# Performance work log

Measured on AMD Instinct MI355X. Metric: run time of the kernel, lower is better.

## Reference

```python
import jax, jax.numpy as jnp
import numpy as np

D_MODEL = 256
NUM_HEADS = 4
D_HEAD = D_MODEL // NUM_HEADS
LN_EPS = 1e-5
NEG_INF = -1e9


def setup_inputs() -> dict:
    key = jax.random.key(0)
    ks = jax.random.split(key, 8)
    B, N = 4, 2048
    s = 1.0 / np.sqrt(D_MODEL)
    return {
        "x": jax.random.normal(ks[0], (B, N, D_MODEL), dtype=jnp.float32),
        "Wq": jax.random.normal(ks[1], (D_MODEL, D_MODEL), dtype=jnp.float32) * s,
        "Wk": jax.random.normal(ks[2], (D_MODEL, D_MODEL), dtype=jnp.float32) * s,
        "Wv": jax.random.normal(ks[3], (D_MODEL, D_MODEL), dtype=jnp.float32) * s,
        "Wo": jax.random.normal(ks[4], (D_MODEL, D_MODEL), dtype=jnp.float32) * s,
        "bo": jnp.zeros((D_MODEL,), dtype=jnp.float32),
        "gamma": jnp.ones((D_MODEL,), dtype=jnp.float32),
        "beta": jnp.zeros((D_MODEL,), dtype=jnp.float32),
        "k_neighbors": 8,
    }


def build_knn_adj(x, k):
    # x: [B, N, D]; returns symmetric 0/1 adjacency [B, N, N]
    B, N, _ = x.shape
    xn = x / jnp.maximum(jnp.linalg.norm(x, axis=-1, keepdims=True), 1e-12)
    sim = jnp.einsum('bnd,bmd->bnm', xn, xn)  # [B, N, N]
    _, idx = jax.lax.top_k(sim, k + 1)        # [B, N, k+1]
    b = jnp.arange(B)[:, None, None]
    r = jnp.arange(N)[None, :, None]
    adj = jnp.zeros((B, N, N), dtype=jnp.float32).at[b, r, idx].add(1.0)
    adj = jnp.maximum(adj, jnp.swapaxes(adj, 1, 2))
    return adj


def layer_norm(x, gamma, beta):
    mu = jnp.mean(x, axis=-1, keepdims=True)
    var = jnp.mean(jnp.square(x - mu), axis=-1, keepdims=True)
    return (x - mu) * jax.lax.rsqrt(var + LN_EPS) * gamma + beta


def reference(x, Wq, Wk, Wv, Wo, bo, gamma, beta, k_neighbors):
    B, N, D = x.shape
    adj = build_knn_adj(x, k_neighbors)  # [B, N, N]

    def split_heads(t):  # [B, N, D] -> [B, H, N, d]
        return jnp.transpose(t.reshape(B, N, NUM_HEADS, D_HEAD), (0, 2, 1, 3))

    q = split_heads(x @ Wq)
    k = split_heads(x @ Wk)
    v = split_heads(x @ Wv)

    scores = jnp.einsum('bhnd,bhmd->bhnm', q, k) / jnp.sqrt(jnp.float32(D_HEAD))
    scores = jnp.where(adj[:, None, :, :] > 0, scores, NEG_INF)
    attn = jax.nn.softmax(scores, axis=-1)  # dropout is identity at inference
    out = jnp.einsum('bhnm,bhmd->bhnd', attn, v)
    out = jnp.transpose(out, (0, 2, 1, 3)).reshape(B, N, D)
    out = out @ Wo + bo
    return layer_norm(x + out, gamma, beta)
```

## Files before the change

kernel.cpp:

```cpp
#include <hip/hip_runtime.h>
#include <hip/hip_bf16.h>
#include <math.h>

#define BATCH 4
#define N 2048
#define D 256
#define NH 4
#define DH 64
#define TOPK 9
#define NEG_BIG -1e30f

typedef __bf16 bf16;
typedef __bf16 bf16x8 __attribute__((ext_vector_type(8)));
typedef float f32x4 __attribute__((ext_vector_type(4)));

#define PK3(a,b,c) ((a) | ((b) << 2) | ((c) << 4))
#define PK6(a,b,c,d,e,f) ((a) | ((b) << 2) | ((c) << 4) | ((d) << 6) | ((e) << 8) | ((f) << 10))

#define WAITVM(Nc) __builtin_amdgcn_s_waitcnt((((Nc) & 0xf)) | (7u << 4) | (0xfu << 8) | ((((unsigned)(Nc)) >> 4) << 14))

__device__ __forceinline__ void async_cp16(const bf16* g, const bf16* l) {
  __builtin_amdgcn_global_load_lds(
      (const __attribute__((address_space(1))) void*)(uintptr_t)g,
      (__attribute__((address_space(3))) void*)(uintptr_t)l, 16, 0, 0);
}

__global__ __launch_bounds__(64) void prep_kernel(const float* __restrict__ x,
                                                  const float* __restrict__ Wq,
                                                  const float* __restrict__ Wk,
                                                  const float* __restrict__ Wv,
                                                  const float* __restrict__ Wo,
                                                  bf16* __restrict__ XsN,
                                                  bf16* __restrict__ Wt,
                                                  float* __restrict__ norms,
                                                  uint4* __restrict__ mask4) {
  int blk = blockIdx.x;
  int lane = threadIdx.x;
  if (blk < 8192) {
    float4 v = *(const float4*)(x + (size_t)blk * D + lane * 4);
    float ss = v.x * v.x + v.y * v.y + v.z * v.z + v.w * v.w;
    for (int off = 32; off; off >>= 1) ss += __shfl_down(ss, off);
    ss = __shfl(ss, 0);
    float nrm = fmaxf(sqrtf(ss), 1e-12f);
    if (lane == 0) norms[blk] = nrm;
    float sc = 1.0f / nrm;
    float xs[4] = {v.x * sc, v.y * sc, v.z * sc, v.w * sc};
    bf16* o = XsN + (size_t)blk * 768 + lane * 4;
#pragma unroll
    for (int j = 0; j < 4; ++j) {
      float xv = xs[j];
      bf16 h = (bf16)xv;
      float r1 = xv - (float)h;
      bf16 m = (bf16)r1;
      o[j] = h;
      o[256 + j] = m;
      o[512 + j] = (bf16)(r1 - (float)m);
    }
  } else if (blk < 9216) {
    int jj = blk - 8192;
    const float* W = (jj < 256) ? Wq : (jj < 512) ? Wk : (jj < 768) ? Wv : Wo;
    int j = jj & 255;
    bf16* dst = Wt + (size_t)jj * 512;
    for (int k = lane; k < 256; k += 64) {
      float w = W[(size_t)k * D + j];
      bf16 h = (bf16)w;
      dst[k] = h;
      dst[256 + k] = (bf16)(w - (float)h);
    }
  } else {
    int base = (blk - 9216) * 1024 + lane;
#pragma unroll
    for (int t = 0; t < 16; ++t)
      mask4[base + t * 64] = make_uint4(0, 0, 0, 0);
  }
}

__device__ __forceinline__ void gemm_core(bf16* As, bf16* Bs,
                                          const bf16* __restrict__ Ab,
                                          const bf16* __restrict__ Bb,
                                          float* __restrict__ Cb,
                                          int lda, int ldb, int ldc,
                                          int nsteps, int amap, int bmap,
                                          int row0, int col0,
                                          bool mirror, bool nt,
                                          const float* __restrict__ rowscale) {
  int tid = threadIdx.x;
  int lane = tid & 63;
  int wv = tid >> 6;
  int wm = (wv >> 1) * 64;
  int wn = (wv & 1) * 64;

  int rbase = tid >> 3;
  int gperm = (tid & 7) ^ (rbase & 7);
  const bf16* ga0 = Ab + (size_t)rbase * lda + gperm * 8;
  const bf16* gb0 = Bb + (size_t)rbase * ldb + gperm * 8;
  int ldsoff = tid * 8;

  int fr = lane & 15;
  int fq = (lane >> 4) * 8;

  f32x4 acc[4][4] = {};

  auto issue = [&](int st, int buf) {
    int ch = st >> 2;
    int aoff = (((amap >> (ch * 2)) & 3) << 8) | ((st & 3) << 6);
    int boff = (((bmap >> (ch * 2)) & 3) << 8) | ((st & 3) << 6);
#pragma unroll
    for (int q = 0; q < 4; ++q)
      async_cp16(ga0 + (size_t)q * 32 * lda + aoff, &As[buf * 8192 + ldsoff + q * 2048]);
#pragma unroll
    for (int q = 0; q < 4; ++q)
      async_cp16(gb0 + (size_t)q * 32 * ldb + boff, &Bs[buf * 8192 + ldsoff + q * 2048]);
  };

  issue(0, 0);
  for (int st = 0; st < nsteps; ++st) {
    int buf = st & 1;
    if (st + 1 < nsteps) {
      issue(st + 1, buf ^ 1);
      WAITVM(8);
    } else {
      WAITVM(0);
    }
    __builtin_amdgcn_s_barrier();
#pragma unroll
    for (int ks = 0; ks < 64; ks += 32) {
      bf16x8 af[4], bfr[4];
#pragma unroll
      for (int mi = 0; mi < 4; ++mi) {
        int r = wm + mi * 16 + fr;
        int G = (ks + fq) >> 3;
        af[mi] = *(const bf16x8*)&As[buf * 8192 + r * 64 + ((G ^ (r & 7)) << 3)];
      }
#pragma unroll
      for (int nj = 0; nj < 4; ++nj) {
        int r = wn + nj * 16 + fr;
        int G = (ks + fq) >> 3;
        bfr[nj] = *(const bf16x8*)&Bs[buf * 8192 + r * 64 + ((G ^ (r & 7)) << 3)];
      }
#pragma unroll
      for (int mi = 0; mi < 4; ++mi)
#pragma unroll
        for (int nj = 0; nj < 4; ++nj)
          acc[mi][nj] = __builtin_amdgcn_mfma_f32_16x16x32_bf16(af[mi], bfr[nj], acc[mi][nj], 0, 0, 0);
    }
    __builtin_amdgcn_s_barrier();
  }

  int er = (lane >> 4) * 4;
  int ec = lane & 15;
#pragma unroll
  for (int mi = 0; mi < 4; ++mi) {
    int rb = row0 + wm + mi * 16 + er;
    float scl[4] = {1.f, 1.f, 1.f, 1.f};
    if (rowscale) {
      float4 s4 = *(const float4*)(rowscale + rb);
      scl[0] = s4.x; scl[1] = s4.y; scl[2] = s4.z; scl[3] = s4.w;
    }
#pragma unroll
    for (int nj = 0; nj < 4; ++nj) {
      int cb = col0 + wn + nj * 16 + ec;
      if (nt) {
#pragma unroll
        for (int reg = 0; reg < 4; ++reg)
          __builtin_nontemporal_store(acc[mi][nj][reg],
                                      &Cb[(size_t)(rb + reg) * ldc + cb]);
        if (mirror) {
#pragma unroll
          for (int reg = 0; reg < 4; ++reg)
            __builtin_nontemporal_store(acc[mi][nj][reg],
                                        &Cb[(size_t)cb * ldc + rb + reg]);
        }
      } else {
#pragma unroll
        for (int reg = 0; reg < 4; ++reg)
          Cb[(size_t)(rb + reg) * ldc + cb] = acc[mi][nj][reg] * scl[reg];
      }
    }
  }
}

__global__ __launch_bounds__(256) void gemm_sim_kernel(const bf16* __restrict__ XsN,
                                                       float* __restrict__ sim,
                                                       int amap, int bmap) {
  __shared__ bf16 As[2 * 128 * 64];
  __shared__ bf16 Bs[2 * 128 * 64];
  int g = blockIdx.x;
  int xcd = g & 7;
  int slot = g >> 3;
  int z = xcd >> 1;
  int t = (xcd & 1) * 68 + slot;
  int by = 0;
  while (t >= 16 - by) { t -= 16 - by; ++by; }
  int bx = by + t;
  gemm_core(As, Bs,
            XsN + (size_t)z * N * 768 + (size_t)by * 128 * 768,
            XsN + (size_t)z * N * 768 + (size_t)bx * 128 * 768,
            sim + (size_t)z * N * N,
            768, 768, N, 12, amap, bmap, by * 128, bx * 128,
            bx != by, true, nullptr);
}

__global__ __launch_bounds__(256) void gemm_gen_kernel(const bf16* __restrict__ A,
                                                       const bf16* __restrict__ B,
                                                       float* __restrict__ C,
                                                       int lda, int ldb, int ldc,
                                                       int nsteps, int amap, int bmap,
                                                       const float* __restrict__ rowscale) {
  __shared__ bf16 As[2 * 128 * 64];
  __shared__ bf16 Bs[2 * 128 * 64];
  gemm_core(As, Bs,
            A + (size_t)blockIdx.y * 128 * lda,
            B + (size_t)blockIdx.x * 128 * ldb,
            C, lda, ldb, ldc, nsteps, amap, bmap,
            blockIdx.y * 128, blockIdx.x * 128, false, false, rowscale);
}

__global__ __launch_bounds__(256) void gemm_fused_kernel(const bf16* __restrict__ XsN,
                                                         float* __restrict__ sim,
                                                         int amap_s, int bmap_s,
                                                         const bf16* __restrict__ Wt,
                                                         float* __restrict__ qkv,
                                                         int amap_q, int bmap_q,
                                                         const float* __restrict__ norms) {
  __shared__ bf16 As[2 * 128 * 64];
  __shared__ bf16 Bs[2 * 128 * 64];
  int g = blockIdx.x;
  if (g < 544) {
    int xcd = g & 7;
    int slot = g >> 3;
    int z = xcd >> 1;
    int t = (xcd & 1) * 68 + slot;
    int by = 0;
    while (t >= 16 - by) { t -= 16 - by; ++by; }
    int bx = by + t;
    gemm_core(As, Bs,
              XsN + (size_t)z * N * 768 + (size_t)by * 128 * 768,
              XsN + (size_t)z * N * 768 + (size_t)bx * 128 * 768,
              sim + (size_t)z * N * N,
              768, 768, N, 12, amap_s, bmap_s, by * 128, bx * 128,
              bx != by, true, nullptr);
  } else {
    int t = g - 544;
    int bx = t % 6;
    int by = t / 6;
    gemm_core(As, Bs,
              XsN + (size_t)by * 128 * 768,
              Wt + (size_t)bx * 128 * 512,
              qkv, 768, 512, 768, 8, amap_q, bmap_q,
              by * 128, bx * 128, false, false, norms);
  }
}

__global__ __launch_bounds__(64) void topk_adj_kernel(const float* __restrict__ sim,
                                                      unsigned* __restrict__ mask) {
  int row = blockIdx.x;
  int lane = threadIdx.x;
  int b = row >> 11, r = row & 2047;
  const float* srow = sim + (size_t)row * N;
  float v[32];
#pragma unroll
  for (int it = 0; it < 8; ++it) {
    float4 q = *(const float4*)(srow + it * 256 + lane * 4);
    v[it * 4 + 0] = q.x; v[it * 4 + 1] = q.y;
    v[it * 4 + 2] = q.z; v[it * 4 + 3] = q.w;
  }
  unsigned removed = 0;
  for (int rs = 0; rs < TOPK; ++rs) {
    float m = -3e38f;
    int mi = 0;
#pragma unroll
    for (int i = 0; i < 32; ++i) {
      float vv = ((removed >> i) & 1u) ? -3e38f : v[i];
      if (vv > m) { m = vv; mi = i; }
    }
    int gidx = ((mi >> 2) << 8) + lane * 4 + (mi & 3);
    for (int off = 32; off; off >>= 1) {
      float om = __shfl_down(m, off);
      int og = __shfl_down(gidx, off);
      if (om > m || (om == m && og < gidx)) { m = om; gidx = og; }
    }
    gidx = __shfl(gidx, 0);
    if (((gidx >> 2) & 63) == lane)
      removed |= 1u << (((gidx >> 8) << 2) | (gidx & 3));
    if (lane == 0) {
      atomicOr(&mask[(size_t)row * 64 + (gidx >> 5)], 1u << (gidx & 31));
      atomicOr(&mask[(((size_t)b << 11) + gidx) * 64 + (r >> 5)], 1u << (r & 31));
    }
  }
}

__global__ __launch_bounds__(256) void attn_kernel(const float* __restrict__ qkv,
                                                   const unsigned* __restrict__ mask,
                                                   bf16* __restrict__ aos) {
  __shared__ float sq[4][256];
  __shared__ unsigned short nbr[4][2048];
  __shared__ int s_nn[4];
  int wv = threadIdx.x >> 6;
  int lane = threadIdx.x & 63;
  int g = blockIdx.x;
  int xcd = g & 7;
  int b = xcd >> 1;
  int tile = (xcd & 1) * 256 + (g >> 3);
  int bn = b * N + tile * 4 + wv;
  if (lane == 0) s_nn[wv] = 0;
  *(float4*)&sq[wv][lane * 4] = *(const float4*)(qkv + (size_t)bn * 768 + lane * 4);
  __syncthreads();
  unsigned bits = mask[(size_t)bn * (N / 32) + lane];
  while (bits) {
    int bit = __ffs(bits) - 1;
    bits &= bits - 1;
    int p = atomicAdd(&s_nn[wv], 1);
    nbr[wv][p] = (unsigned short)(lane * 32 + bit);
  }
  __syncthreads();
  int nn = s_nn[wv];
  const float* base = qkv + (size_t)b * N * 768;
  float acc[4] = {0.f, 0.f, 0.f, 0.f};

  auto score4 = [&](int j, float* s) {
    const float* kr = base + (size_t)j * 768 + 256;
#pragma unroll
    for (int h = 0; h < 4; ++h) {
      float a = 0.f;
#pragma unroll
      for (int c = 0; c < DH; c += 4) {
        float4 kk = *(const float4*)(kr + h * DH + c);
        a += sq[wv][h * DH + c] * kk.x + sq[wv][h * DH + c + 1] * kk.y +
             sq[wv][h * DH + c + 2] * kk.z + sq[wv][h * DH + c + 3] * kk.w;
      }
      s[h] = a * 0.125f;
    }
  };

  if (nn <= 64) {
    float s[4] = {NEG_BIG, NEG_BIG, NEG_BIG, NEG_BIG};
    if (lane < nn) score4(nbr[wv][lane], s);
    float w[4], l[4];
#pragma unroll
    for (int h = 0; h < 4; ++h) {
      float m = s[h];
      for (int off = 32; off; off >>= 1) m = fmaxf(m, __shfl_down(m, off));
      m = __shfl(m, 0);
      float e = (lane < nn) ? __expf(s[h] - m) : 0.f;
      float ls = e;
      for (int off = 32; off; off >>= 1) ls += __shfl_down(ls, off);
      l[h] = __shfl(ls, 0);
      w[h] = e;
    }
    int i = 0;
    for (; i + 4 <= nn; i += 4) {
      int j0 = nbr[wv][i + 0], j1 = nbr[wv][i + 1];
      int j2 = nbr[wv][i + 2], j3 = nbr[wv][i + 3];
      const float* p0 = base + (size_t)j0 * 768 + 512;
      const float* p1 = base + (size_t)j1 * 768 + 512;
      const float* p2 = base + (size_t)j2 * 768 + 512;
      const float* p3 = base + (size_t)j3 * 768 + 512;
#pragma unroll
      for (int h = 0; h < 4; ++h) {
        acc[h] += __shfl(w[h], i + 0) * p0[h * DH + lane] +
                  __shfl(w[h], i + 1) * p1[h * DH + lane] +
                  __shfl(w[h], i + 2) * p2[h * DH + lane] +
                  __shfl(w[h], i + 3) * p3[h * DH + lane];
      }
    }
    for (; i < nn; ++i) {
      const float* p0 = base + (size_t)nbr[wv][i] * 768 + 512;
#pragma unroll
      for (int h = 0; h < 4; ++h) acc[h] += __shfl(w[h], i) * p0[h * DH + lane];
    }
#pragma unroll
    for (int h = 0; h < 4; ++h) acc[h] /= l[h];
  } else {
    float m[4] = {NEG_BIG, NEG_BIG, NEG_BIG, NEG_BIG};
    for (int i0 = 0; i0 < nn; i0 += 64) {
      float s[4] = {NEG_BIG, NEG_BIG, NEG_BIG, NEG_BIG};
      if (i0 + lane < nn) score4(nbr[wv][i0 + lane], s);
#pragma unroll
      for (int h = 0; h < 4; ++h) m[h] = fmaxf(m[h], s[h]);
    }
#pragma unroll
    for (int h = 0; h < 4; ++h) {
      for (int off = 32; off; off >>= 1) m[h] = fmaxf(m[h], __shfl_down(m[h], off));
      m[h] = __shfl(m[h], 0);
    }
    float l[4] = {0.f, 0.f, 0.f, 0.f};
    for (int i0 = 0; i0 < nn; i0 += 64) {
      float s[4] = {NEG_BIG, NEG_BIG, NEG_BIG, NEG_BIG};
      if (i0 + lane < nn) score4(nbr[wv][i0 + lane], s);
      float e[4];
#pragma unroll
      for (int h = 0; h < 4; ++h) {
        e[h] = (i0 + lane < nn) ? __expf(s[h] - m[h]) : 0.f;
        float ls = e[h];
        for (int off = 32; off; off >>= 1) ls += __shfl_down(ls, off);
        l[h] += __shfl(ls, 0);
      }
      int lim = min(64, nn - i0);
      for (int ii = 0; ii < lim; ++ii) {
        const float* p0 = base + (size_t)nbr[wv][i0 + ii] * 768 + 512;
#pragma unroll
        for (int h = 0; h < 4; ++h) acc[h] += __shfl(e[h], ii) * p0[h * DH + lane];
      }
    }
#pragma unroll
    for (int h = 0; h < 4; ++h) acc[h] /= l[h];
  }
#pragma unroll
  for (int h = 0; h < 4; ++h) {
    float a = acc[h];
    bf16 hi = (bf16)a;
    aos[(size_t)bn * 512 + h * DH + lane] = hi;
    aos[(size_t)bn * 512 + 256 + h * DH + lane] = (bf16)(a - (float)hi);
  }
}

__global__ __launch_bounds__(64) void ln_kernel(const float* __restrict__ x,
                                                const float* __restrict__ proj,
                                                const float* __restrict__ bo,
                                                const float* __restrict__ gamma,
                                                const float* __restrict__ beta,
                                                float* __restrict__ out) {
  int row = blockIdx.x;
  int lane = threadIdx.x;
  size_t base = (size_t)row * D + lane * 4;
  float4 xv = *(const float4*)(x + base);
  float4 pv = *(const float4*)(proj + base);
  float4 bv = *(const float4*)(bo + lane * 4);
  float u0 = xv.x + pv.x + bv.x, u1 = xv.y + pv.y + bv.y;
  float u2 = xv.z + pv.z + bv.z, u3 = xv.w + pv.w + bv.w;
  float s = u0 + u1 + u2 + u3;
  for (int off = 32; off; off >>= 1) s += __shfl_down(s, off);
  s = __shfl(s, 0);
  float mean = s * (1.0f / D);
  float d0 = u0 - mean, d1 = u1 - mean, d2 = u2 - mean, d3 = u3 - mean;
  float ss = d0 * d0 + d1 * d1 + d2 * d2 + d3 * d3;
  for (int off = 32; off; off >>= 1) ss += __shfl_down(ss, off);
  ss = __shfl(ss, 0);
  float rstd = rsqrtf(ss * (1.0f / D) + 1e-5f);
  float4 gv = *(const float4*)(gamma + lane * 4);
  float4 be = *(const float4*)(beta + lane * 4);
  float4 o;
  o.x = d0 * rstd * gv.x + be.x;
  o.y = d1 * rstd * gv.y + be.y;
  o.z = d2 * rstd * gv.z + be.z;
  o.w = d3 * rstd * gv.w + be.w;
  *(float4*)(out + base) = o;
}

extern "C" void kernel_launch(void* const* d_in, const int* in_sizes, int n_in,
                              void* d_out, int out_size, void* d_ws, size_t ws_size,
                              hipStream_t stream) {
  const float* x     = (const float*)d_in[0];
  const float* Wq    = (const float*)d_in[1];
  const float* Wk    = (const float*)d_in[2];
  const float* Wv    = (const float*)d_in[3];
  const float* Wo    = (const float*)d_in[4];
  const float* bo    = (const float*)d_in[5];
  const float* gamma = (const float*)d_in[6];
  const float* beta  = (const float*)d_in[7];
  float* out = (float*)d_out;

  char* ws = (char*)d_ws;
  bf16* XsN      = (bf16*)(ws);
  float* sim     = (float*)(ws + 12582912);
  float* norms   = (float*)(ws + 79691776);
  unsigned* mask = (unsigned*)(ws + 79986688);
  bf16* Wt       = (bf16*)(ws + 82083840);

  bool big = ws_size >= (size_t)125075456;
  float* qkv  = (float*)(ws + (big ? 83132416  : 12582912));
  bf16* aos   = (bf16*)(ws + (big ? 108298240 : 37748736));
  float* proj = (float*)(ws + (big ? 116686848 : 46137344));

  const int AMAP_SIM = PK6(0, 0, 1, 0, 0, 0);
  const int BMAP_SIM = PK6(0, 1, 0, 0, 0, 0);
  const int AMAP_2T  = PK3(0, 1, 0);
  const int BMAP_2T  = PK3(0, 0, 1);

  prep_kernel<<<9344, 64, 0, stream>>>(x, Wq, Wk, Wv, Wo, XsN, Wt, norms,
                                       (uint4*)mask);

  if (big) {
    gemm_fused_kernel<<<928, 256, 0, stream>>>(
        XsN, sim, AMAP_SIM, BMAP_SIM, Wt, qkv, AMAP_2T, BMAP_2T, norms);
    topk_adj_kernel<<<BATCH * N, 64, 0, stream>>>(sim, mask);
  } else {
    gemm_sim_kernel<<<544, 256, 0, stream>>>(XsN, sim, AMAP_SIM, BMAP_SIM);
    topk_adj_kernel<<<BATCH * N, 64, 0, stream>>>(sim, mask);
    gemm_gen_kernel<<<dim3(6, 64), 256, 0, stream>>>(
        XsN, Wt, qkv, 768, 512, 768, 8, AMAP_2T, BMAP_2T, norms);
  }

  attn_kernel<<<(BATCH * N) / 4, 256, 0, stream>>>(qkv, mask, aos);

  gemm_gen_kernel<<<dim3(2, 64), 256, 0, stream>>>(
      aos, Wt + (size_t)768 * 512, proj, 512, 512, D, 8, AMAP_2T, BMAP_2T, nullptr);
  ln_kernel<<<BATCH * N, 64, 0, stream>>>(x, proj, bo, gamma, beta, out);
}
```

Before: 198.7 us.

## Store QKV in bf16, shrink the normalized-x split, and fuse out-projection with LayerNorm

The normalized-x representation drops from a three-term bf16 split to a two-term split. That shrinks the buffer and its stride, though the sim GEMM keeps its step count. The QKV GEMM now writes bf16 instead of fp32, which halves the gather traffic in the attention kernel, where K and V are converted on load. The output projection GEMM and the LayerNorm kernel are merged into one projln kernel. Each block computes a full 128x256 row tile and reduces the row statistics in LDS, so the fp32 proj intermediate and one launch disappear. In exchange, precision drops for the similarity scores, which can change top-k selection, and for Q/K/V. The fused kernel also launches only 64 blocks, which leaves most compute units idle.

```diff
diff --git a/kernel.cpp b/kernel.cpp
--- a/kernel.cpp
+++ b/kernel.cpp
@@ -11,6 +11,7 @@
 #define NEG_BIG -1e30f
 
 typedef __bf16 bf16;
+typedef __bf16 bf16x4 __attribute__((ext_vector_type(4)));
 typedef __bf16 bf16x8 __attribute__((ext_vector_type(8)));
 typedef float f32x4 __attribute__((ext_vector_type(4)));
 
@@ -45,16 +46,13 @@
     if (lane == 0) norms[blk] = nrm;
     float sc = 1.0f / nrm;
     float xs[4] = {v.x * sc, v.y * sc, v.z * sc, v.w * sc};
-    bf16* o = XsN + (size_t)blk * 768 + lane * 4;
+    bf16* o = XsN + (size_t)blk * 512 + lane * 4;
 #pragma unroll
     for (int j = 0; j < 4; ++j) {
       float xv = xs[j];
       bf16 h = (bf16)xv;
-      float r1 = xv - (float)h;
-      bf16 m = (bf16)r1;
       o[j] = h;
-      o[256 + j] = m;
-      o[512 + j] = (bf16)(r1 - (float)m);
+      o[256 + j] = (bf16)(xv - (float)h);
     }
   } else if (blk < 9216) {
     int jj = blk - 8192;
@@ -78,11 +76,11 @@
 __device__ __forceinline__ void gemm_core(bf16* As, bf16* Bs,
                                           const bf16* __restrict__ Ab,
                                           const bf16* __restrict__ Bb,
-                                          float* __restrict__ Cb,
+                                          void* __restrict__ Cvoid,
                                           int lda, int ldb, int ldc,
                                           int nsteps, int amap, int bmap,
                                           int row0, int col0,
-                                          bool mirror, bool nt,
+                                          int outmode, bool mirror,
                                           const float* __restrict__ rowscale) {
   int tid = threadIdx.x;
   int lane = tid & 63;
@@ -160,7 +158,8 @@
 #pragma unroll
     for (int nj = 0; nj < 4; ++nj) {
       int cb = col0 + wn + nj * 16 + ec;
-      if (nt) {
+      if (outmode == 1) {
+        float* Cb = (float*)Cvoid;
 #pragma unroll
         for (int reg = 0; reg < 4; ++reg)
           __builtin_nontemporal_store(acc[mi][nj][reg],
@@ -172,9 +171,10 @@
                                         &Cb[(size_t)cb * ldc + rb + reg]);
         }
       } else {
+        bf16* Cb = (bf16*)Cvoid;
 #pragma unroll
         for (int reg = 0; reg < 4; ++reg)
-          Cb[(size_t)(rb + reg) * ldc + cb] = acc[mi][nj][reg] * scl[reg];
+          Cb[(size_t)(rb + reg) * ldc + cb] = (bf16)(acc[mi][nj][reg] * scl[reg]);
       }
     }
   }
@@ -194,33 +194,32 @@
   while (t >= 16 - by) { t -= 16 - by; ++by; }
   int bx = by + t;
   gemm_core(As, Bs,
-            XsN + (size_t)z * N * 768 + (size_t)by * 128 * 768,
-            XsN + (size_t)z * N * 768 + (size_t)bx * 128 * 768,
+            XsN + (size_t)z * N * 512 + (size_t)by * 128 * 512,
+            XsN + (size_t)z * N * 512 + (size_t)bx * 128 * 512,
             sim + (size_t)z * N * N,
-            768, 768, N, 12, amap, bmap, by * 128, bx * 128,
-            bx != by, true, nullptr);
-}
-
-__global__ __launch_bounds__(256) void gemm_gen_kernel(const bf16* __restrict__ A,
-                                                       const bf16* __restrict__ B,
-                                                       float* __restrict__ C,
-                                                       int lda, int ldb, int ldc,
-                                                       int nsteps, int amap, int bmap,
-                                                       const float* __restrict__ rowscale) {
+            512, 512, N, 12, amap, bmap, by * 128, bx * 128,
+            1, bx != by, nullptr);
+}
+
+__global__ __launch_bounds__(256) void gemm_qkv_kernel(const bf16* __restrict__ XsN,
+                                                       const bf16* __restrict__ Wt,
+                                                       bf16* __restrict__ qkv,
+                                                       int amap, int bmap,
+                                                       const float* __restrict__ norms) {
   __shared__ bf16 As[2 * 128 * 64];
   __shared__ bf16 Bs[2 * 128 * 64];
   gemm_core(As, Bs,
-            A + (size_t)blockIdx.y * 128 * lda,
-            B + (size_t)blockIdx.x * 128 * ldb,
-            C, lda, ldb, ldc, nsteps, amap, bmap,
-            blockIdx.y * 128, blockIdx.x * 128, false, false, rowscale);
+            XsN + (size_t)blockIdx.y * 128 * 512,
+            Wt + (size_t)blockIdx.x * 128 * 512,
+            qkv, 512, 512, 768, 8, amap, bmap,
+            blockIdx.y * 128, blockIdx.x * 128, 2, false, norms);
 }
 
 __global__ __launch_bounds__(256) void gemm_fused_kernel(const bf16* __restrict__ XsN,
                                                          float* __restrict__ sim,
                                                          int amap_s, int bmap_s,
                                                          const bf16* __restrict__ Wt,
-                                                         float* __restrict__ qkv,
+                                                         bf16* __restrict__ qkv,
                                                          int amap_q, int bmap_q,
                                                          const float* __restrict__ norms) {
   __shared__ bf16 As[2 * 128 * 64];
@@ -235,20 +234,20 @@
     while (t >= 16 - by) { t -= 16 - by; ++by; }
     int bx = by + t;
     gemm_core(As, Bs,
-              XsN + (size_t)z * N * 768 + (size_t)by * 128 * 768,
-              XsN + (size_t)z * N * 768 + (size_t)bx * 128 * 768,
+              XsN + (size_t)z * N * 512 + (size_t)by * 128 * 512,
+              XsN + (size_t)z * N * 512 + (size_t)bx * 128 * 512,
               sim + (size_t)z * N * N,
-              768, 768, N, 12, amap_s, bmap_s, by * 128, bx * 128,
-              bx != by, true, nullptr);
+              512, 512, N, 12, amap_s, bmap_s, by * 128, bx * 128,
+              1, bx != by, nullptr);
   } else {
     int t = g - 544;
     int bx = t % 6;
     int by = t / 6;
     gemm_core(As, Bs,
-              XsN + (size_t)by * 128 * 768,
+              XsN + (size_t)by * 128 * 512,
               Wt + (size_t)bx * 128 * 512,
-              qkv, 768, 512, 768, 8, amap_q, bmap_q,
-              by * 128, bx * 128, false, false, norms);
+              qkv, 512, 512, 768, 8, amap_q, bmap_q,
+              by * 128, bx * 128, 2, false, norms);
   }
 }
 
@@ -290,7 +289,7 @@
   }
 }
 
-__global__ __launch_bounds__(256) void attn_kernel(const float* __restrict__ qkv,
+__global__ __launch_bounds__(256) void attn_kernel(const bf16* __restrict__ qkv,
                                                    const unsigned* __restrict__ mask,
                                                    bf16* __restrict__ aos) {
   __shared__ float sq[4][256];
@@ -304,7 +303,11 @@
   int tile = (xcd & 1) * 256 + (g >> 3);
   int bn = b * N + tile * 4 + wv;
   if (lane == 0) s_nn[wv] = 0;
-  *(float4*)&sq[wv][lane * 4] = *(const float4*)(qkv + (size_t)bn * 768 + lane * 4);
+  {
+    bf16x4 qv = *(const bf16x4*)(qkv + (size_t)bn * 768 + lane * 4);
+#pragma unroll
+    for (int j = 0; j < 4; ++j) sq[wv][lane * 4 + j] = (float)qv[j];
+  }
   __syncthreads();
   unsigned bits = mask[(size_t)bn * (N / 32) + lane];
   while (bits) {
@@ -315,19 +318,19 @@
   }
   __syncthreads();
   int nn = s_nn[wv];
-  const float* base = qkv + (size_t)b * N * 768;
+  const bf16* base = qkv + (size_t)b * N * 768;
   float acc[4] = {0.f, 0.f, 0.f, 0.f};
 
   auto score4 = [&](int j, float* s) {
-    const float* kr = base + (size_t)j * 768 + 256;
+    const bf16* kr = base + (size_t)j * 768 + 256;
 #pragma unroll
     for (int h = 0; h < 4; ++h) {
       float a = 0.f;
 #pragma unroll
-      for (int c = 0; c < DH; c += 4) {
-        float4 kk = *(const float4*)(kr + h * DH + c);
-        a += sq[wv][h * DH + c] * kk.x + sq[wv][h * DH + c + 1] * kk.y +
-             sq[wv][h * DH + c + 2] * kk.z + sq[wv][h * DH + c + 3] * kk.w;
+      for (int c = 0; c < DH; c += 8) {
+        bf16x8 kk = *(const bf16x8*)(kr + h * DH + c);
+#pragma unroll
+        for (int t = 0; t < 8; ++t) a += sq[wv][h * DH + c + t] * (float)kk[t];
       }
       s[h] = a * 0.125f;
     }
@@ -352,22 +355,22 @@
     for (; i + 4 <= nn; i += 4) {
       int j0 = nbr[wv][i + 0], j1 = nbr[wv][i + 1];
       int j2 = nbr[wv][i + 2], j3 = nbr[wv][i + 3];
-      const float* p0 = base + (size_t)j0 * 768 + 512;
-      const float* p1 = base + (size_t)j1 * 768 + 512;
-      const float* p2 = base + (size_t)j2 * 768 + 512;
-      const float* p3 = base + (size_t)j3 * 768 + 512;
+      const bf16* p0 = base + (size_t)j0 * 768 + 512;
+      const bf16* p1 = base + (size_t)j1 * 768 + 512;
+      const bf16* p2 = base + (size_t)j2 * 768 + 512;
+      const bf16* p3 = base + (size_t)j3 * 768 + 512;
 #pragma unroll
       for (int h = 0; h < 4; ++h) {
-        acc[h] += __shfl(w[h], i + 0) * p0[h * DH + lane] +
-                  __shfl(w[h], i + 1) * p1[h * DH + lane] +
-                  __shfl(w[h], i + 2) * p2[h * DH + lane] +
-                  __shfl(w[h], i + 3) * p3[h * DH + lane];
+        acc[h] += __shfl(w[h], i + 0) * (float)p0[h * DH + lane] +
+                  __shfl(w[h], i + 1) * (float)p1[h * DH + lane] +
+                  __shfl(w[h], i + 2) * (float)p2[h * DH + lane] +
+                  __shfl(w[h], i + 3) * (float)p3[h * DH + lane];
       }
     }
     for (; i < nn; ++i) {
-      const float* p0 = base + (size_t)nbr[wv][i] * 768 + 512;
-#pragma unroll
-      for (int h = 0; h < 4; ++h) acc[h] += __shfl(w[h], i) * p0[h * DH + lane];
+      const bf16* p0 = base + (size_t)nbr[wv][i] * 768 + 512;
+#pragma unroll
+      for (int h = 0; h < 4; ++h) acc[h] += __shfl(w[h], i) * (float)p0[h * DH + lane];
     }
 #pragma unroll
     for (int h = 0; h < 4; ++h) acc[h] /= l[h];
@@ -398,9 +401,9 @@
       }
       int lim = min(64, nn - i0);
       for (int ii = 0; ii < lim; ++ii) {
-        const float* p0 = base + (size_t)nbr[wv][i0 + ii] * 768 + 512;
-#pragma unroll
-        for (int h = 0; h < 4; ++h) acc[h] += __shfl(e[h], ii) * p0[h * DH + lane];
+        const bf16* p0 = base + (size_t)nbr[wv][i0 + ii] * 768 + 512;
+#pragma unroll
+        for (int h = 0; h < 4; ++h) acc[h] += __shfl(e[h], ii) * (float)p0[h * DH + lane];
       }
     }
 #pragma unroll
@@ -415,37 +418,120 @@
   }
 }
 
-__global__ __launch_bounds__(64) void ln_kernel(const float* __restrict__ x,
-                                                const float* __restrict__ proj,
-                                                const float* __restrict__ bo,
-                                                const float* __restrict__ gamma,
-                                                const float* __restrict__ beta,
-                                                float* __restrict__ out) {
-  int row = blockIdx.x;
-  int lane = threadIdx.x;
-  size_t base = (size_t)row * D + lane * 4;
-  float4 xv = *(const float4*)(x + base);
-  float4 pv = *(const float4*)(proj + base);
-  float4 bv = *(const float4*)(bo + lane * 4);
-  float u0 = xv.x + pv.x + bv.x, u1 = xv.y + pv.y + bv.y;
-  float u2 = xv.z + pv.z + bv.z, u3 = xv.w + pv.w + bv.w;
-  float s = u0 + u1 + u2 + u3;
-  for (int off = 32; off; off >>= 1) s += __shfl_down(s, off);
-  s = __shfl(s, 0);
-  float mean = s * (1.0f / D);
-  float d0 = u0 - mean, d1 = u1 - mean, d2 = u2 - mean, d3 = u3 - mean;
-  float ss = d0 * d0 + d1 * d1 + d2 * d2 + d3 * d3;
-  for (int off = 32; off; off >>= 1) ss += __shfl_down(ss, off);
-  ss = __shfl(ss, 0);
-  float rstd = rsqrtf(ss * (1.0f / D) + 1e-5f);
-  float4 gv = *(const float4*)(gamma + lane * 4);
-  float4 be = *(const float4*)(beta + lane * 4);
-  float4 o;
-  o.x = d0 * rstd * gv.x + be.x;
-  o.y = d1 * rstd * gv.y + be.y;
-  o.z = d2 * rstd * gv.z + be.z;
-  o.w = d3 * rstd * gv.w + be.w;
-  *(float4*)(out + base) = o;
+__global__ __launch_bounds__(256) void projln_kernel(const bf16* __restrict__ A,
+                                                     const bf16* __restrict__ Bw,
+                                                     const float* __restrict__ x,
+                                                     const float* __restrict__ bo,
+                                                     const float* __restrict__ gamma,
+                                                     const float* __restrict__ beta,
+                                                     float* __restrict__ out) {
+  __shared__ bf16 As[2 * 128 * 32];
+  __shared__ bf16 Bs[2 * 256 * 32];
+  __shared__ float rsum[128][2];
+  __shared__ float rsq[128][2];
+  int tid = threadIdx.x;
+  int lane = tid & 63;
+  int wv = tid >> 6;
+  int wm = (wv >> 1) * 64;
+  int wn = (wv & 1) * 128;
+  int row0 = blockIdx.x * 128;
+
+  int rt = tid >> 2;
+  int gperm = (tid & 3) ^ ((rt >> 1) & 3);
+  const bf16* ga0 = A + (size_t)(row0 + rt) * 512 + gperm * 8;
+  const bf16* gb0 = Bw + (size_t)rt * 512 + gperm * 8;
+
+  int fr = lane & 15;
+  int G = lane >> 4;
+
+  f32x4 acc[4][8] = {};
+
+  auto issue = [&](int st, int buf) {
+    int aoff = ((st >> 3) << 8) | ((st & 7) << 5);
+    int boff = (st & 7) << 5;
+#pragma unroll
+    for (int q = 0; q < 2; ++q)
+      async_cp16(ga0 + (size_t)q * 64 * 512 + aoff, &As[buf * 4096 + tid * 8 + q * 2048]);
+#pragma unroll
+    for (int q = 0; q < 4; ++q)
+      async_cp16(gb0 + (size_t)q * 64 * 512 + boff, &Bs[buf * 8192 + tid * 8 + q * 2048]);
+  };
+
+  issue(0, 0);
+  for (int st = 0; st < 16; ++st) {
+    int buf = st & 1;
+    if (st + 1 < 16) {
+      issue(st + 1, buf ^ 1);
+      WAITVM(6);
+    } else {
+      WAITVM(0);
+    }
+    __builtin_amdgcn_s_barrier();
+    bf16x8 af[4], bfr[8];
+#pragma unroll
+    for (int mi = 0; mi < 4; ++mi) {
+      int r = wm + mi * 16 + fr;
+      af[mi] = *(const bf16x8*)&As[buf * 4096 + r * 32 + ((G ^ ((r >> 1) & 3)) << 3)];
+    }
+#pragma unroll
+    for (int nj = 0; nj < 8; ++nj) {
+      int r = wn + nj * 16 + fr;
+      bfr[nj] = *(const bf16x8*)&Bs[buf * 8192 + r * 32 + ((G ^ ((r >> 1) & 3)) << 3)];
+    }
+#pragma unroll
+    for (int mi = 0; mi < 4; ++mi)
+#pragma unroll
+      for (int nj = 0; nj < 8; ++nj)
+        acc[mi][nj] = __builtin_amdgcn_mfma_f32_16x16x32_bf16(af[mi], bfr[nj], acc[mi][nj], 0, 0, 0);
+    __builtin_amdgcn_s_barrier();
+  }
+
+  int er = (lane >> 4) * 4;
+  int ec = lane & 15;
+  float bo_c[8], ga_c[8], be_c[8];
+#pragma unroll
+  for (int nj = 0; nj < 8; ++nj) {
+    int c = wn + nj * 16 + ec;
+    bo_c[nj] = bo[c]; ga_c[nj] = gamma[c]; be_c[nj] = beta[c];
+  }
+#pragma unroll
+  for (int mi = 0; mi < 4; ++mi)
+#pragma unroll
+    for (int reg = 0; reg < 4; ++reg) {
+      int rloc = wm + mi * 16 + er + reg;
+      const float* xr = x + (size_t)(row0 + rloc) * D;
+      float su = 0.f, s2 = 0.f;
+#pragma unroll
+      for (int nj = 0; nj < 8; ++nj) {
+        float u = acc[mi][nj][reg] + bo_c[nj] + xr[wn + nj * 16 + ec];
+        su += u; s2 += u * u;
+      }
+#pragma unroll
+      for (int m = 1; m <= 8; m <<= 1) {
+        su += __shfl_xor(su, m);
+        s2 += __shfl_xor(s2, m);
+      }
+      if (ec == 0) { rsum[rloc][wv & 1] = su; rsq[rloc][wv & 1] = s2; }
+    }
+  __syncthreads();
+#pragma unroll
+  for (int mi = 0; mi < 4; ++mi)
+#pragma unroll
+    for (int reg = 0; reg < 4; ++reg) {
+      int rloc = wm + mi * 16 + er + reg;
+      float s = rsum[rloc][0] + rsum[rloc][1];
+      float q2 = rsq[rloc][0] + rsq[rloc][1];
+      float mean = s * (1.0f / D);
+      float var = q2 * (1.0f / D) - mean * mean;
+      float rstd = rsqrtf(var + 1e-5f);
+      const float* xr = x + (size_t)(row0 + rloc) * D;
+      float* orow = out + (size_t)(row0 + rloc) * D;
+#pragma unroll
+      for (int nj = 0; nj < 8; ++nj) {
+        float u = acc[mi][nj][reg] + bo_c[nj] + xr[wn + nj * 16 + ec];
+        orow[wn + nj * 16 + ec] = (u - mean) * rstd * ga_c[nj] + be_c[nj];
+      }
+    }
 }
 
 extern "C" void kernel_launch(void* const* d_in, const int* in_sizes, int n_in,
@@ -468,10 +554,9 @@
   unsigned* mask = (unsigned*)(ws + 79986688);
   bf16* Wt       = (bf16*)(ws + 82083840);
 
-  bool big = ws_size >= (size_t)125075456;
-  float* qkv  = (float*)(ws + (big ? 83132416  : 12582912));
-  bf16* aos   = (bf16*)(ws + (big ? 108298240 : 37748736));
-  float* proj = (float*)(ws + (big ? 116686848 : 46137344));
+  bool big = ws_size >= (size_t)125000000;
+  bf16* qkv = (bf16*)(ws + (big ? 83132416 : 12582912));
+  bf16* aos = (bf16*)(ws + (big ? 95715328 : 37748736));
 
   const int AMAP_SIM = PK6(0, 0, 1, 0, 0, 0);
   const int BMAP_SIM = PK6(0, 1, 0, 0, 0, 0);
@@ -488,13 +573,12 @@
   } else {
     gemm_sim_kernel<<<544, 256, 0, stream>>>(XsN, sim, AMAP_SIM, BMAP_SIM);
     topk_adj_kernel<<<BATCH * N, 64, 0, stream>>>(sim, mask);
-    gemm_gen_kernel<<<dim3(6, 64), 256, 0, stream>>>(
-        XsN, Wt, qkv, 768, 512, 768, 8, AMAP_2T, BMAP_2T, norms);
+    gemm_qkv_kernel<<<dim3(6, 64), 256, 0, stream>>>(XsN, Wt, qkv,
+                                                     AMAP_2T, BMAP_2T, norms);
   }
 
   attn_kernel<<<(BATCH * N) / 4, 256, 0, stream>>>(qkv, mask, aos);
 
-  gemm_gen_kernel<<<dim3(2, 64), 256, 0, stream>>>(
-      aos, Wt + (size_t)768 * 512, proj, 512, 512, D, 8, AMAP_2T, BMAP_2T, nullptr);
-  ln_kernel<<<BATCH * N, 64, 0, stream>>>(x, proj, bo, gamma, beta, out);
-}
+  projln_kernel<<<64, 256, 0, stream>>>(aos, Wt + (size_t)768 * 512,
+                                        x, bo, gamma, beta, out);
+}
```

After: 199.7 us. Within noise of the previous version (+0.5%).
